# Performance work log

Measured on AMD Instinct MI355X. Metric: run time of the kernel, lower is better.

## Reference

```python
import jax, jax.numpy as jnp
import numpy as np
import math

D = 768
H = 8
DK = D // H
FF = 1024
EPS = 1e-5


def _layer_norm(x, g, b):
    m = jnp.mean(x, axis=-1, keepdims=True)
    v = jnp.mean((x - m) ** 2, axis=-1, keepdims=True)
    return (x - m) * jax.lax.rsqrt(v + EPS) * g + b


def _mha(x, attention_mask, Wq, bq, Wv, bv, g, b):
    # x: (B,S,D); attention_mask: (B,S,1) bool (True = masked/padding query row)
    B, S, _ = x.shape
    q = (x @ Wq + bq).reshape(B, S, H, DK).transpose(0, 2, 1, 3)  # (B,H,S,dk)
    # NOTE: original code uses the V projection for BOTH k and v (k = self.V(x))
    kv = (x @ Wv + bv).reshape(B, S, H, DK).transpose(0, 2, 1, 3)
    k = kv
    v = kv
    w = jnp.einsum('bhqd,bhkd->bhqk', q, k) / math.sqrt(DK)  # (B,H,S,S)
    pad = attention_mask[:, None, :, :]                      # (B,1,S,1) -> bcast (B,1,S,S)
    causal = jnp.triu(jnp.ones((S, S), dtype=bool), k=1)     # look-ahead mask
    mask = pad | causal
    w = jnp.where(mask, jnp.float32(-1e9), w)
    # NOTE: original uses nn.Softmax(dim=2) -> softmax over the QUERY axis
    score = jax.nn.softmax(w, axis=2)
    o = jnp.einsum('bhqk,bhkd->bhqd', score, v)              # (B,H,S,dk)
    o = o.transpose(0, 2, 1, 3).reshape(B, S, D)
    return _layer_norm(o + x, g, b)


def _ffn(x, W1, b1, W2, b2, g, b):
    h = jax.nn.relu(x @ W1 + b1)
    return _layer_norm(h @ W2 + b2 + x, g, b)


def setup_inputs() -> dict:
    key = jax.random.key(0)
    ks = jax.random.split(key, 16)
    B, S = 8, 1024
    sc = 0.02
    inp = {
        'x': jax.random.normal(ks[0], (B, S, D), dtype=jnp.float32),
        'attention_mask': jax.random.randint(ks[1], (B, S, 1), 0, 2).astype(bool),
    }
    for i, pre in enumerate(['a1', 'a2']):
        inp[pre + '_Wq'] = jax.random.normal(ks[2 + 4 * i], (D, D), dtype=jnp.float32) * sc
        inp[pre + '_bq'] = jnp.zeros((D,), dtype=jnp.float32)
        inp[pre + '_Wv'] = jax.random.normal(ks[3 + 4 * i], (D, D), dtype=jnp.float32) * sc
        inp[pre + '_bv'] = jnp.zeros((D,), dtype=jnp.float32)
        inp[pre + '_g'] = jnp.ones((D,), dtype=jnp.float32)
        inp[pre + '_b'] = jnp.zeros((D,), dtype=jnp.float32)
    inp['f_W1'] = jax.random.normal(ks[10], (D, FF), dtype=jnp.float32) * sc
    inp['f_b1'] = jnp.zeros((FF,), dtype=jnp.float32)
    inp['f_W2'] = jax.random.normal(ks[11], (FF, D), dtype=jnp.float32) * sc
    inp['f_b2'] = jnp.zeros((D,), dtype=jnp.float32)
    inp['f_g'] = jnp.ones((D,), dtype=jnp.float32)
    inp['f_b'] = jnp.zeros((D,), dtype=jnp.float32)
    return inp


def reference(x, attention_mask,
              a1_Wq, a1_bq, a1_Wv, a1_bv, a1_g, a1_b,
              a2_Wq, a2_bq, a2_Wv, a2_bv, a2_g, a2_b,
              f_W1, f_b1, f_W2, f_b2, f_g, f_b):
    x = _mha(x, attention_mask, a1_Wq, a1_bq, a1_Wv, a1_bv, a1_g, a1_b)
    x = _mha(x, attention_mask, a2_Wq, a2_bq, a2_Wv, a2_bv, a2_g, a2_b)
    x = _ffn(x, f_W1, f_b1, f_W2, f_b2, f_g, f_b)
    return x
```

## Files before the change

kernel.cpp:

```cpp
#include <hip/hip_runtime.h>
#include <cstddef>

#define BB 8
#define SS 1024
#define DD 768
#define HH 8
#define DKK 96
#define FFF 1024
#define MM (BB*SS)
#define QVW 1536
#define SM_SCALE 0.10206207261596577f
#define NT2 8

typedef unsigned short ushort_t;
typedef short short8 __attribute__((ext_vector_type(8)));
typedef float f32x4 __attribute__((ext_vector_type(4)));
typedef float f32x16 __attribute__((ext_vector_type(16)));
typedef ushort_t us4 __attribute__((ext_vector_type(4)));
typedef unsigned uint2v __attribute__((ext_vector_type(2)));

__device__ __forceinline__ ushort_t f2b(float f) {
    union { float f; unsigned u; } x; x.f = f;
    unsigned r = x.u + 0x7fffu + ((x.u >> 16) & 1u);
    return (ushort_t)(r >> 16);
}
__device__ __forceinline__ float b2f(ushort_t u) {
    union { unsigned u; float f; } x; x.u = ((unsigned)u) << 16;
    return x.f;
}
__device__ __forceinline__ void gload16(const ushort_t* g, void* lds_base) {
    __builtin_amdgcn_global_load_lds(
        (const __attribute__((address_space(1))) unsigned int*)g,
        (__attribute__((address_space(3))) unsigned int*)lds_base, 16, 0, 0);
}
__device__ __forceinline__ void plswap(unsigned& a, unsigned& b) {
#if __has_builtin(__builtin_amdgcn_permlane32_swap)
    uint2v r = __builtin_amdgcn_permlane32_swap(a, b, false, false);
    a = r[0]; b = r[1];
#else
    asm("v_permlane32_swap_b32 %0, %1" : "+v"(a), "+v"(b));
#endif
}

__global__ __launch_bounds__(256) void castWT(
    const float* __restrict__ W, ushort_t* __restrict__ Wt, int K, int N)
{
    __shared__ float T[32][33];
    const int tx = threadIdx.x & 31, ty = threadIdx.x >> 5;
    const int n0 = blockIdx.x * 32, k0 = blockIdx.y * 32;
    #pragma unroll
    for (int r = 0; r < 4; ++r)
        T[ty + 8*r][tx] = W[(size_t)(k0 + ty + 8*r) * N + n0 + tx];
    __syncthreads();
    #pragma unroll
    for (int r = 0; r < 4; ++r)
        Wt[(size_t)(n0 + ty + 8*r) * K + k0 + tx] = f2b(T[tx][ty + 8*r]);
}

__global__ __launch_bounds__(256) void castWT4(
    const float* __restrict__ Wa, const float* __restrict__ Wb,
    const float* __restrict__ Wc, const float* __restrict__ Wd,
    ushort_t* __restrict__ Ta, ushort_t* __restrict__ Tb,
    ushort_t* __restrict__ Tc, ushort_t* __restrict__ Td)
{
    __shared__ float T[32][33];
    const float* W; ushort_t* Wt;
    switch (blockIdx.z) {
        case 0:  W = Wa; Wt = Ta; break;
        case 1:  W = Wb; Wt = Tb; break;
        case 2:  W = Wc; Wt = Tc; break;
        default: W = Wd; Wt = Td; break;
    }
    const int tx = threadIdx.x & 31, ty = threadIdx.x >> 5;
    const int n0 = blockIdx.x * 32, k0 = blockIdx.y * 32;
    #pragma unroll
    for (int r = 0; r < 4; ++r)
        T[ty + 8*r][tx] = W[(size_t)(k0 + ty + 8*r) * DD + n0 + tx];
    __syncthreads();
    #pragma unroll
    for (int r = 0; r < 4; ++r)
        Wt[(size_t)(n0 + ty + 8*r) * DD + k0 + tx] = f2b(T[tx][ty + 8*r]);
}

__global__ __launch_bounds__(256) void cast_f2b(
    const float* __restrict__ in, ushort_t* __restrict__ out, int n4)
{
    const int i = blockIdx.x * 256 + threadIdx.x;
    if (i >= n4) return;
    const float4 v = ((const float4*)in)[i];
    us4 o; o.x = f2b(v.x); o.y = f2b(v.y); o.z = f2b(v.z); o.w = f2b(v.w);
    ((us4*)out)[i] = o;
}

template<int RELU>
__global__ __launch_bounds__(256) void gemm_bt(
    const ushort_t* __restrict__ A, const ushort_t* __restrict__ Bt,
    const float* __restrict__ bias, const float* __restrict__ bias2, int bN,
    ushort_t* __restrict__ C, int K, int N)
{
    __shared__ ushort_t S[128*136];
    ushort_t* As = S;
    ushort_t* Bs = S + 128*64;
    const int tid  = threadIdx.x;
    const int lane = tid & 63, wave = tid >> 6;
    const int wm = wave >> 1, wn = wave & 1;
    const int n = lane & 15, quad = lane >> 4;
    const int sx = n & 7;
    const int bm = blockIdx.y * 128, bn = blockIdx.x * 128;

    f32x4 acc[4][4];
    #pragma unroll
    for (int i = 0; i < 4; ++i)
        #pragma unroll
        for (int j = 0; j < 4; ++j) acc[i][j] = (f32x4){0.f, 0.f, 0.f, 0.f};

    for (int k0 = 0; k0 < K; k0 += 64) {
        #pragma unroll
        for (int it = 0; it < 4; ++it) {
            const int u   = (it*4 + wave)*64 + lane;
            const int row = u >> 3;
            const int c   = (u & 7) ^ (row & 7);
            gload16(A  + (size_t)(bm + row) * K + k0 + c*8, (char*)As + (it*4 + wave)*1024);
            gload16(Bt + (size_t)(bn + row) * K + k0 + c*8, (char*)Bs + (it*4 + wave)*1024);
        }
        __syncthreads();
        #pragma unroll
        for (int ks = 0; ks < 2; ++ks) {
            short8 af[4], bf[4];
            #pragma unroll
            for (int i = 0; i < 4; ++i)
                af[i] = *(short8*)&As[((wm*64 + i*16 + n)*8 + ((ks*4 + quad) ^ sx))*8];
            #pragma unroll
            for (int j = 0; j < 4; ++j)
                bf[j] = *(short8*)&Bs[((wn*64 + j*16 + n)*8 + ((ks*4 + quad) ^ sx))*8];
            #pragma unroll
            for (int i = 0; i < 4; ++i)
                #pragma unroll
                for (int j = 0; j < 4; ++j)
                    acc[i][j] = __builtin_amdgcn_mfma_f32_16x16x32_bf16(af[i], bf[j], acc[i][j], 0, 0, 0);
        }
        __syncthreads();
    }
    #pragma unroll
    for (int j = 0; j < 4; ++j) {
        const int col = wn*64 + j*16 + n;
        const int gcol = bn + col;
        const float bsv = (gcol < bN) ? bias[gcol] : bias2[gcol - bN];
        #pragma unroll
        for (int i = 0; i < 4; ++i) {
            const int lrow = wm*64 + i*16 + quad*4;
            #pragma unroll
            for (int r = 0; r < 4; ++r) {
                float v = acc[i][j][r] + bsv;
                if (RELU) v = fmaxf(v, 0.f);
                S[(lrow + r)*136 + col] = f2b(v);
            }
        }
    }
    __syncthreads();
    #pragma unroll
    for (int it = 0; it < 8; ++it) {
        const int u = it*256 + tid;
        const int grow = u >> 4, gc = u & 15;
        *(short8*)(C + (size_t)(bm + grow)*N + bn + gc*8) = *(short8*)&S[grow*136 + gc*8];
    }
}

__global__ __launch_bounds__(512) void attn_sums(
    const ushort_t* __restrict__ QV, const int* __restrict__ amask,
    float* __restrict__ lpart)
{
    __shared__ ushort_t Qs[128*128];
    __shared__ ushort_t Ks[2][64*128];
    __shared__ float colsum[2][8][64];
    const int tid = threadIdx.x, lane = tid & 63, wave = tid >> 6;
    const int n = lane & 15, quad = lane >> 4, sx = n & 7;
    const int hwid = blockIdx.x;
    const int v = (hwid & 7) * 32 + (hwid >> 3);
    const int px = v & 3, h = (v >> 2) & 7, b = v >> 5;
    const ushort_t* Qh = QV + (size_t)b*SS*QVW + h*DKK;
    const ushort_t* Kh = QV + (size_t)b*SS*QVW + DD + h*DKK;
    float* lpq = lpart + (size_t)(b*HH + h)*NT2*SS;

    #pragma unroll
    for (int half = 0; half < 2; ++half) {
        const int qt2 = half ? (7 - px) : px;
        const int q0 = qt2 * 128;
        const int ktmax = 2*qt2 + 1;
        #pragma unroll
        for (int it = 0; it < 4; ++it) {
            const int u = (it*8 + wave)*64 + lane;
            const int row = u >> 4, c = (u & 15) ^ (row & 7);
            if (c < 12)
                gload16(Qh + (size_t)(q0 + row)*QVW + c*8, (char*)Qs + (it*8 + wave)*1024);
        }
        const int4 mv = *(const int4*)&amask[b*SS + q0 + wave*16 + quad*4];
        const int mr[4] = {mv.x, mv.y, mv.z, mv.w};
        #pragma unroll
        for (int it = 0; it < 2; ++it) {
            const int u = (it*8 + wave)*64 + lane;
            const int row = u >> 4, c = (u & 15) ^ (row & 7);
            if (c < 12)
                gload16(Kh + (size_t)row*QVW + c*8, (char*)Ks[0] + (it*8 + wave)*1024);
        }
        __syncthreads();
        short8 aq[3];
        #pragma unroll
        for (int ks = 0; ks < 3; ++ks)
            aq[ks] = *(short8*)&Qs[((wave*16 + n)*16 + ((ks*4 + quad) ^ sx))*8];

        int cur = 0;
        for (int kt = 0; kt <= ktmax; ++kt) {
            const int k0 = kt * 64;
            if (kt < ktmax) {
                #pragma unroll
                for (int it = 0; it < 2; ++it) {
                    const int u = (it*8 + wave)*64 + lane;
                    const int row = u >> 4, c = (u & 15) ^ (row & 7);
                    if (c < 12)
                        gload16(Kh + (size_t)(k0 + 64 + row)*QVW + c*8,
                                (char*)Ks[cur^1] + (it*8 + wave)*1024);
                }
            }
            if (kt > 0 && tid < 64) {
                const float s = colsum[cur^1][0][tid] + colsum[cur^1][1][tid]
                              + colsum[cur^1][2][tid] + colsum[cur^1][3][tid]
                              + colsum[cur^1][4][tid] + colsum[cur^1][5][tid]
                              + colsum[cur^1][6][tid] + colsum[cur^1][7][tid];
                lpq[(size_t)qt2*SS + (k0 - 64) + tid] = s;
            }
            #pragma unroll
            for (int ns = 0; ns < 4; ++ns) {
                f32x4 sa = (f32x4){0.f, 0.f, 0.f, 0.f};
                #pragma unroll
                for (int ks = 0; ks < 3; ++ks) {
                    const short8 bk = *(short8*)&Ks[cur][((ns*16 + n)*16 + ((ks*4 + quad) ^ sx))*8];
                    sa = __builtin_amdgcn_mfma_f32_16x16x32_bf16(aq[ks], bk, sa, 0, 0, 0);
                }
                const int kl = ns*16 + n;
                const int keyg = k0 + kl;
                float s = 0.f;
                #pragma unroll
                for (int r = 0; r < 4; ++r) {
                    const int qg = q0 + wave*16 + quad*4 + r;
                    const bool dead = (mr[r] != 0) || (keyg > qg);
                    s += dead ? 0.f : __expf(sa[r] * SM_SCALE);
                }
                s += __shfl_xor(s, 16);
                s += __shfl_xor(s, 32);
                if (quad == 0) colsum[cur][wave][kl] = s;
            }
            __syncthreads();
            cur ^= 1;
        }
        if (tid < 64) {
            const int pb = ktmax & 1;
            const float s = colsum[pb][0][tid] + colsum[pb][1][tid]
                          + colsum[pb][2][tid] + colsum[pb][3][tid]
                          + colsum[pb][4][tid] + colsum[pb][5][tid]
                          + colsum[pb][6][tid] + colsum[pb][7][tid];
            lpq[(size_t)qt2*SS + ktmax*64 + tid] = s;
        }
    }
}

__global__ __launch_bounds__(256) void transpose_scale(
    const ushort_t* __restrict__ QV, const float* __restrict__ lpart,
    ushort_t* __restrict__ Vt)
{
    __shared__ ushort_t T[64][104];
    __shared__ float rlv[64];
    const int tid = threadIdx.x;
    const int k0 = blockIdx.x * 64, h = blockIdx.y, b = blockIdx.z;
    const ushort_t* src = QV + (size_t)b*SS*QVW + DD + h*DKK;
    for (int s = tid; s < 768; s += 256) {
        const int r = s / 12, c = s % 12;
        *(short8*)&T[r][c*8] = *(const short8*)(src + (size_t)(k0 + r)*QVW + c*8);
    }
    if (tid < 64) {
        const float* lp = lpart + (size_t)(b*HH + h)*NT2*SS;
        float l = 0.f;
        for (int qt2 = k0 >> 7; qt2 < NT2; ++qt2) l += lp[(size_t)qt2*SS + k0 + tid];
        rlv[tid] = (l > 0.f) ? (1.f / l) : 0.f;
    }
    __syncthreads();
    ushort_t* dst = Vt + ((size_t)b*HH + h)*DKK*SS;
    for (int s = tid; s < 768; s += 256) {
        const int dk = s >> 3, c = s & 7;
        short8 v;
        #pragma unroll
        for (int i = 0; i < 8; ++i)
            v[i] = (short)f2b(b2f(T[c*8 + i][dk]) * rlv[c*8 + i]);
        *(short8*)(dst + (size_t)dk*SS + k0 + c*8) = v;
    }
}

__global__ __launch_bounds__(256, 2) void attn_pv_re(
    const ushort_t* __restrict__ QV, const int* __restrict__ amask,
    const ushort_t* __restrict__ Vt, ushort_t* __restrict__ O)
{
    __shared__ ushort_t Ks[2][64*128];
    __shared__ ushort_t Vs[2][96*64];
    const int tid = threadIdx.x, lane = tid & 63, wave = tid >> 6;
    const int ln31 = lane & 31, hi = lane >> 5;
    const int hwid = blockIdx.x;
    const int v = (hwid & 7) * 32 + (hwid >> 3);
    const int px = v & 3, h = (v >> 2) & 7, b = v >> 5;
    const ushort_t* Qh = QV + (size_t)b*SS*QVW + h*DKK;
    const ushort_t* Kh = QV + (size_t)b*SS*QVW + DD + h*DKK;
    const ushort_t* Vth = Vt + ((size_t)b*HH + h)*DKK*SS;

    #pragma unroll
    for (int half = 0; half < 2; ++half) {
        const int qt2 = half ? (7 - px) : px;
        const int q0 = qt2 * 128;
        const int ktmax = 2*qt2 + 1;
        const int qrow = q0 + wave*32 + ln31;
        short8 bq[6];
        #pragma unroll
        for (int t = 0; t < 6; ++t)
            bq[t] = *(const short8*)(Qh + (size_t)qrow*QVW + t*16 + hi*8);
        const bool padq = amask[b*SS + qrow] != 0;

        #pragma unroll
        for (int it = 0; it < 4; ++it) {
            const int u = (it*4 + wave)*64 + lane;
            const int row = u >> 4, c = (u & 15) ^ (row & 7);
            if (c < 12)
                gload16(Kh + (size_t)row*QVW + c*8, (char*)Ks[0] + (it*4 + wave)*1024);
        }
        #pragma unroll
        for (int it = 0; it < 3; ++it) {
            const int u = (it*4 + wave)*64 + lane;
            const int row = u >> 3, c = (u & 7) ^ (row & 7);
            gload16(Vth + (size_t)row*SS + c*8, (char*)Vs[0] + (it*4 + wave)*1024);
        }
        __syncthreads();

        f32x16 acc[3];
        #pragma unroll
        for (int db = 0; db < 3; ++db)
            #pragma unroll
            for (int i = 0; i < 16; ++i) acc[db][i] = 0.f;

        int cur = 0;
        for (int kt = 0; kt <= ktmax; ++kt) {
            const int k0 = kt * 64;
            if (kt < ktmax) {
                #pragma unroll
                for (int it = 0; it < 4; ++it) {
                    const int u = (it*4 + wave)*64 + lane;
                    const int row = u >> 4, c = (u & 15) ^ (row & 7);
                    if (c < 12)
                        gload16(Kh + (size_t)(k0 + 64 + row)*QVW + c*8,
                                (char*)Ks[cur^1] + (it*4 + wave)*1024);
                }
                #pragma unroll
                for (int it = 0; it < 3; ++it) {
                    const int u = (it*4 + wave)*64 + lane;
                    const int row = u >> 3, c = (u & 7) ^ (row & 7);
                    gload16(Vth + (size_t)row*SS + k0 + 64 + c*8,
                            (char*)Vs[cur^1] + (it*4 + wave)*1024);
                }
            }
            #pragma unroll
            for (int kb = 0; kb < 2; ++kb) {
                f32x16 sk;
                #pragma unroll
                for (int i = 0; i < 16; ++i) sk[i] = 0.f;
                const int krow = kb*32 + ln31;
                #pragma unroll
                for (int t = 0; t < 6; ++t) {
                    const short8 ak = *(short8*)&Ks[cur][krow*128 + (((t*2 + hi) ^ (krow & 7))*8)];
                    sk = __builtin_amdgcn_mfma_f32_32x32x16_bf16(ak, bq[t], sk, 0, 0, 0);
                }
                const int kbase = k0 + kb*32 + 4*hi;
                float p[16];
                #pragma unroll
                for (int r = 0; r < 16; ++r) {
                    const int kg = kbase + (r & 3) + 8*(r >> 2);
                    const bool dead = padq || (kg > qrow);
                    p[r] = dead ? 0.f : __expf(sk[r] * SM_SCALE);
                }
                unsigned w[8];
                #pragma unroll
                for (int i = 0; i < 8; ++i)
                    asm("v_cvt_pk_bf16_f32 %0, %1, %2" : "=v"(w[i]) : "v"(p[2*i]), "v"(p[2*i+1]));
                plswap(w[0], w[2]);
                plswap(w[1], w[3]);
                plswap(w[4], w[6]);
                plswap(w[5], w[7]);
                #pragma unroll
                for (int s = 0; s < 2; ++s) {
                    short8 ae;
                    unsigned* aeu = (unsigned*)&ae;
                    aeu[0] = w[s*4 + 0]; aeu[1] = w[s*4 + 1];
                    aeu[2] = w[s*4 + 2]; aeu[3] = w[s*4 + 3];
                    #pragma unroll
                    for (int db = 0; db < 3; ++db) {
                        const int drow = db*32 + ln31;
                        const short8 bv = *(short8*)&Vs[cur][drow*64 + (((kb*4 + s*2 + hi) ^ (drow & 7))*8)];
                        acc[db] = __builtin_amdgcn_mfma_f32_32x32x16_bf16(ae, bv, acc[db], 0, 0, 0);
                    }
                }
            }
            __syncthreads();
            cur ^= 1;
        }
        #pragma unroll
        for (int db = 0; db < 3; ++db) {
            #pragma unroll
            for (int r = 0; r < 16; ++r) {
                const int q = q0 + wave*32 + (r & 3) + 8*(r >> 2) + 4*hi;
                O[((size_t)b*SS + q)*DD + h*DKK + db*32 + ln31] = f2b(acc[db][r]);
            }
        }
    }
}

__device__ __forceinline__ float block_sum256(float s, float* tmp4)
{
    #pragma unroll
    for (int off = 32; off > 0; off >>= 1) s += __shfl_down(s, off);
    __syncthreads();
    if ((threadIdx.x & 63) == 0) tmp4[threadIdx.x >> 6] = s;
    __syncthreads();
    return tmp4[0] + tmp4[1] + tmp4[2] + tmp4[3];
}

template<int XBF, int RBF, int OUTF32>
__global__ __launch_bounds__(256) void resid_ln(
    const void* __restrict__ X, const void* __restrict__ R,
    const float* __restrict__ g, const float* __restrict__ beta,
    ushort_t* __restrict__ OutB, float* __restrict__ OutF)
{
    __shared__ float tmp4[4];
    const int row = blockIdx.x;
    const int tid = threadIdx.x;
    float v[3], s = 0.f;
    #pragma unroll
    for (int i = 0; i < 3; ++i) {
        const size_t idx = (size_t)row * DD + tid + 256*i;
        const float xv = XBF ? b2f(((const ushort_t*)X)[idx]) : ((const float*)X)[idx];
        const float rv = RBF ? b2f(((const ushort_t*)R)[idx]) : ((const float*)R)[idx];
        v[i] = xv + rv;
        s += v[i];
    }
    const float mu = block_sum256(s, tmp4) * (1.f / DD);
    float qv = 0.f;
    #pragma unroll
    for (int i = 0; i < 3; ++i) { const float d = v[i] - mu; qv += d * d; }
    const float inv = rsqrtf(block_sum256(qv, tmp4) * (1.f / DD) + 1e-5f);
    #pragma unroll
    for (int i = 0; i < 3; ++i) {
        const int c = tid + 256*i;
        const float o = (v[i] - mu) * inv * g[c] + beta[c];
        if (OUTF32) OutF[(size_t)row * DD + c] = o;
        else        OutB[(size_t)row * DD + c] = f2b(o);
    }
}

extern "C" void kernel_launch(void* const* d_in, const int* in_sizes, int n_in,
                              void* d_out, int out_size, void* d_ws, size_t ws_size,
                              hipStream_t stream)
{
    (void)in_sizes; (void)n_in; (void)out_size; (void)ws_size;
    const float* x0    = (const float*)d_in[0];
    const int*   amask = (const int*)d_in[1];
    const float* a1_Wq = (const float*)d_in[2];
    const float* a1_bq = (const float*)d_in[3];
    const float* a1_Wv = (const float*)d_in[4];
    const float* a1_bv = (const float*)d_in[5];
    const float* a1_g  = (const float*)d_in[6];
    const float* a1_b  = (const float*)d_in[7];
    const float* a2_Wq = (const float*)d_in[8];
    const float* a2_bq = (const float*)d_in[9];
    const float* a2_Wv = (const float*)d_in[10];
    const float* a2_bv = (const float*)d_in[11];
    const float* a2_g  = (const float*)d_in[12];
    const float* a2_b  = (const float*)d_in[13];
    const float* f_W1  = (const float*)d_in[14];
    const float* f_b1  = (const float*)d_in[15];
    const float* f_W2  = (const float*)d_in[16];
    const float* f_b2  = (const float*)d_in[17];
    const float* f_g   = (const float*)d_in[18];
    const float* f_b   = (const float*)d_in[19];

    char* ws = (char*)d_ws;
    size_t off = 0;
    auto alloc = [&](size_t bytes) { void* p = ws + off; off += (bytes + 255) & ~(size_t)255; return p; };
    ushort_t* WqvT1 = (ushort_t*)alloc((size_t)QVW*DD*2);
    ushort_t* WqvT2 = (ushort_t*)alloc((size_t)QVW*DD*2);
    ushort_t* W1T   = (ushort_t*)alloc((size_t)DD*FFF*2);
    ushort_t* W2T   = (ushort_t*)alloc((size_t)DD*FFF*2);
    ushort_t* xb0   = (ushort_t*)alloc((size_t)MM*DD*2);
    ushort_t* xb1   = (ushort_t*)alloc((size_t)MM*DD*2);
    ushort_t* xb2   = (ushort_t*)alloc((size_t)MM*DD*2);
    ushort_t* Ob    = (ushort_t*)alloc((size_t)MM*DD*2);
    ushort_t* QVb   = (ushort_t*)alloc((size_t)MM*QVW*2);
    ushort_t* hb    = QVb;
    ushort_t* Vtb   = (ushort_t*)alloc((size_t)MM*DD*2);
    float* lpart = (float*)alloc((size_t)BB*HH*NT2*SS*4);
    float* out = (float*)d_out;

    const dim3 blk(256);
    const dim3 blk512(512);
    const dim3 gat(256);
    const dim3 gtr(SS/64, HH, BB);
    const dim3 gqv(QVW/128, MM/128);
    const dim3 gf1(FFF/128, MM/128);
    const dim3 gf2(DD/128, MM/128);

    castWT4<<<dim3(DD/32, DD/32, 4), blk, 0, stream>>>(
        a1_Wq, a1_Wv, a2_Wq, a2_Wv,
        WqvT1, WqvT1 + (size_t)DD*DD, WqvT2, WqvT2 + (size_t)DD*DD);
    castWT<<<dim3(FFF/32, DD/32), blk, 0, stream>>>(f_W1, W1T, DD, FFF);
    castWT<<<dim3(DD/32, FFF/32), blk, 0, stream>>>(f_W2, W2T, FFF, DD);
    cast_f2b<<<(MM*DD/4 + 255)/256, blk, 0, stream>>>(x0, xb0, MM*DD/4);

    gemm_bt<0><<<gqv, blk, 0, stream>>>(xb0, WqvT1, a1_bq, a1_bv, DD, QVb, DD, QVW);
    attn_sums<<<gat, blk512, 0, stream>>>(QVb, amask, lpart);
    transpose_scale<<<gtr, blk, 0, stream>>>(QVb, lpart, Vtb);
    attn_pv_re<<<gat, blk, 0, stream>>>(QVb, amask, Vtb, Ob);
    resid_ln<1,0,0><<<dim3(MM), blk, 0, stream>>>(Ob, x0, a1_g, a1_b, xb1, nullptr);

    gemm_bt<0><<<gqv, blk, 0, stream>>>(xb1, WqvT2, a2_bq, a2_bv, DD, QVb, DD, QVW);
    attn_sums<<<gat, blk512, 0, stream>>>(QVb, amask, lpart);
    transpose_scale<<<gtr, blk, 0, stream>>>(QVb, lpart, Vtb);
    attn_pv_re<<<gat, blk, 0, stream>>>(QVb, amask, Vtb, Ob);
    resid_ln<1,1,0><<<dim3(MM), blk, 0, stream>>>(Ob, xb1, a2_g, a2_b, xb2, nullptr);

    gemm_bt<1><<<gf1, blk, 0, stream>>>(xb2, W1T, f_b1, f_b1, FFF, hb, DD, FFF);
    gemm_bt<0><<<gf2, blk, 0, stream>>>(hb, W2T, f_b2, f_b2, DD, Ob, FFF, DD);
    resid_ln<1,1,1><<<dim3(MM), blk, 0, stream>>>(Ob, xb2, f_g, f_b, nullptr, out);
}
```

Measured before the change: 409.0 us.

## Merge prep kernels, swizzle GEMM block order across XCDs, raise MFMA priority

Folds the four weight/input cast kernels into one launch, saving launch gaps. GEMMs switch to a 1D grid remapped so consecutive tiles land on the same XCD, aiming at better L2 reuse of A/B panels. MFMA sections in the GEMM and both attention kernels are wrapped in s_setprio to favour matrix issue over other waves. Together these are independent tweaks whose benefits are modest and depend on scheduling behaviour.

Measured after the change: 382.7 us. 6.4% less time.

```diff
diff --git a/kernel.cpp b/kernel.cpp
--- a/kernel.cpp
+++ b/kernel.cpp
@@ -42,12 +42,13 @@
 #endif
 }
 
-__global__ __launch_bounds__(256) void castWT(
-    const float* __restrict__ W, ushort_t* __restrict__ Wt, int K, int N)
+__device__ __forceinline__ void castWT_body(
+    const float* __restrict__ W, ushort_t* __restrict__ Wt,
+    int K, int N, int bx, int by)
 {
     __shared__ float T[32][33];
     const int tx = threadIdx.x & 31, ty = threadIdx.x >> 5;
-    const int n0 = blockIdx.x * 32, k0 = blockIdx.y * 32;
+    const int n0 = bx * 32, k0 = by * 32;
     #pragma unroll
     for (int r = 0; r < 4; ++r)
         T[ty + 8*r][tx] = W[(size_t)(k0 + ty + 8*r) * N + n0 + tx];
@@ -57,39 +58,33 @@
         Wt[(size_t)(n0 + ty + 8*r) * K + k0 + tx] = f2b(T[tx][ty + 8*r]);
 }
 
-__global__ __launch_bounds__(256) void castWT4(
-    const float* __restrict__ Wa, const float* __restrict__ Wb,
-    const float* __restrict__ Wc, const float* __restrict__ Wd,
-    ushort_t* __restrict__ Ta, ushort_t* __restrict__ Tb,
-    ushort_t* __restrict__ Tc, ushort_t* __restrict__ Td)
-{
-    __shared__ float T[32][33];
-    const float* W; ushort_t* Wt;
-    switch (blockIdx.z) {
-        case 0:  W = Wa; Wt = Ta; break;
-        case 1:  W = Wb; Wt = Tb; break;
-        case 2:  W = Wc; Wt = Tc; break;
-        default: W = Wd; Wt = Td; break;
-    }
-    const int tx = threadIdx.x & 31, ty = threadIdx.x >> 5;
-    const int n0 = blockIdx.x * 32, k0 = blockIdx.y * 32;
-    #pragma unroll
-    for (int r = 0; r < 4; ++r)
-        T[ty + 8*r][tx] = W[(size_t)(k0 + ty + 8*r) * DD + n0 + tx];
-    __syncthreads();
-    #pragma unroll
-    for (int r = 0; r < 4; ++r)
-        Wt[(size_t)(n0 + ty + 8*r) * DD + k0 + tx] = f2b(T[tx][ty + 8*r]);
-}
-
-__global__ __launch_bounds__(256) void cast_f2b(
-    const float* __restrict__ in, ushort_t* __restrict__ out, int n4)
-{
-    const int i = blockIdx.x * 256 + threadIdx.x;
-    if (i >= n4) return;
-    const float4 v = ((const float4*)in)[i];
-    us4 o; o.x = f2b(v.x); o.y = f2b(v.y); o.z = f2b(v.z); o.w = f2b(v.w);
-    ((us4*)out)[i] = o;
+__global__ __launch_bounds__(256) void prep_all(
+    const float* __restrict__ Wqa, const float* __restrict__ Wva,
+    const float* __restrict__ Wqb, const float* __restrict__ Wvb,
+    ushort_t* __restrict__ Tqa, ushort_t* __restrict__ Tva,
+    ushort_t* __restrict__ Tqb, ushort_t* __restrict__ Tvb,
+    const float* __restrict__ W1, ushort_t* __restrict__ T1,
+    const float* __restrict__ W2, ushort_t* __restrict__ T2,
+    const float* __restrict__ x, ushort_t* __restrict__ xb)
+{
+    const int id = blockIdx.x;
+    if (id < 2304) {
+        const int z = id / 576, r = id % 576;
+        const float* W = (z == 0) ? Wqa : (z == 1) ? Wva : (z == 2) ? Wqb : Wvb;
+        ushort_t* Wt   = (z == 0) ? Tqa : (z == 1) ? Tva : (z == 2) ? Tqb : Tvb;
+        castWT_body(W, Wt, DD, DD, r % 24, r / 24);
+    } else if (id < 3072) {
+        const int r = id - 2304;
+        castWT_body(W1, T1, DD, FFF, r % 32, r / 32);
+    } else if (id < 3840) {
+        const int r = id - 3072;
+        castWT_body(W2, T2, FFF, DD, r % 24, r / 24);
+    } else {
+        const int i = (id - 3840) * 256 + threadIdx.x;
+        const float4 v = ((const float4*)x)[i];
+        us4 o; o.x = f2b(v.x); o.y = f2b(v.y); o.z = f2b(v.z); o.w = f2b(v.w);
+        ((us4*)xb)[i] = o;
+    }
 }
 
 template<int RELU>
@@ -106,7 +101,10 @@
     const int wm = wave >> 1, wn = wave & 1;
     const int n = lane & 15, quad = lane >> 4;
     const int sx = n & 7;
-    const int bm = blockIdx.y * 128, bn = blockIdx.x * 128;
+    const int nbx = N >> 7;
+    const int cpx = gridDim.x >> 3;
+    const int sw  = (blockIdx.x & 7) * cpx + (blockIdx.x >> 3);
+    const int bm = (sw / nbx) * 128, bn = (sw % nbx) * 128;
 
     f32x4 acc[4][4];
     #pragma unroll
@@ -133,11 +131,13 @@
             #pragma unroll
             for (int j = 0; j < 4; ++j)
                 bf[j] = *(short8*)&Bs[((wn*64 + j*16 + n)*8 + ((ks*4 + quad) ^ sx))*8];
+            __builtin_amdgcn_s_setprio(1);
             #pragma unroll
             for (int i = 0; i < 4; ++i)
                 #pragma unroll
                 for (int j = 0; j < 4; ++j)
                     acc[i][j] = __builtin_amdgcn_mfma_f32_16x16x32_bf16(af[i], bf[j], acc[i][j], 0, 0, 0);
+            __builtin_amdgcn_s_setprio(0);
         }
         __syncthreads();
     }
@@ -232,11 +232,13 @@
             #pragma unroll
             for (int ns = 0; ns < 4; ++ns) {
                 f32x4 sa = (f32x4){0.f, 0.f, 0.f, 0.f};
+                __builtin_amdgcn_s_setprio(1);
                 #pragma unroll
                 for (int ks = 0; ks < 3; ++ks) {
                     const short8 bk = *(short8*)&Ks[cur][((ns*16 + n)*16 + ((ks*4 + quad) ^ sx))*8];
                     sa = __builtin_amdgcn_mfma_f32_16x16x32_bf16(aq[ks], bk, sa, 0, 0, 0);
                 }
+                __builtin_amdgcn_s_setprio(0);
                 const int kl = ns*16 + n;
                 const int keyg = k0 + kl;
                 float s = 0.f;
@@ -369,11 +371,13 @@
                 #pragma unroll
                 for (int i = 0; i < 16; ++i) sk[i] = 0.f;
                 const int krow = kb*32 + ln31;
+                __builtin_amdgcn_s_setprio(1);
                 #pragma unroll
                 for (int t = 0; t < 6; ++t) {
                     const short8 ak = *(short8*)&Ks[cur][krow*128 + (((t*2 + hi) ^ (krow & 7))*8)];
                     sk = __builtin_amdgcn_mfma_f32_32x32x16_bf16(ak, bq[t], sk, 0, 0, 0);
                 }
+                __builtin_amdgcn_s_setprio(0);
                 const int kbase = k0 + kb*32 + 4*hi;
                 float p[16];
                 #pragma unroll
@@ -390,6 +394,7 @@
                 plswap(w[1], w[3]);
                 plswap(w[4], w[6]);
                 plswap(w[5], w[7]);
+                __builtin_amdgcn_s_setprio(1);
                 #pragma unroll
                 for (int s = 0; s < 2; ++s) {
                     short8 ae;
@@ -403,6 +408,7 @@
                         acc[db] = __builtin_amdgcn_mfma_f32_32x32x16_bf16(ae, bv, acc[db], 0, 0, 0);
                     }
                 }
+                __builtin_amdgcn_s_setprio(0);
             }
             __syncthreads();
             cur ^= 1;
@@ -507,30 +513,25 @@
     const dim3 blk512(512);
     const dim3 gat(256);
     const dim3 gtr(SS/64, HH, BB);
-    const dim3 gqv(QVW/128, MM/128);
-    const dim3 gf1(FFF/128, MM/128);
-    const dim3 gf2(DD/128, MM/128);
-
-    castWT4<<<dim3(DD/32, DD/32, 4), blk, 0, stream>>>(
+
+    prep_all<<<dim3(9984), blk, 0, stream>>>(
         a1_Wq, a1_Wv, a2_Wq, a2_Wv,
-        WqvT1, WqvT1 + (size_t)DD*DD, WqvT2, WqvT2 + (size_t)DD*DD);
-    castWT<<<dim3(FFF/32, DD/32), blk, 0, stream>>>(f_W1, W1T, DD, FFF);
-    castWT<<<dim3(DD/32, FFF/32), blk, 0, stream>>>(f_W2, W2T, FFF, DD);
-    cast_f2b<<<(MM*DD/4 + 255)/256, blk, 0, stream>>>(x0, xb0, MM*DD/4);
-
-    gemm_bt<0><<<gqv, blk, 0, stream>>>(xb0, WqvT1, a1_bq, a1_bv, DD, QVb, DD, QVW);
+        WqvT1, WqvT1 + (size_t)DD*DD, WqvT2, WqvT2 + (size_t)DD*DD,
+        f_W1, W1T, f_W2, W2T, x0, xb0);
+
+    gemm_bt<0><<<dim3((QVW/128)*(MM/128)), blk, 0, stream>>>(xb0, WqvT1, a1_bq, a1_bv, DD, QVb, DD, QVW);
     attn_sums<<<gat, blk512, 0, stream>>>(QVb, amask, lpart);
     transpose_scale<<<gtr, blk, 0, stream>>>(QVb, lpart, Vtb);
     attn_pv_re<<<gat, blk, 0, stream>>>(QVb, amask, Vtb, Ob);
     resid_ln<1,0,0><<<dim3(MM), blk, 0, stream>>>(Ob, x0, a1_g, a1_b, xb1, nullptr);
 
-    gemm_bt<0><<<gqv, blk, 0, stream>>>(xb1, WqvT2, a2_bq, a2_bv, DD, QVb, DD, QVW);
+    gemm_bt<0><<<dim3((QVW/128)*(MM/128)), blk, 0, stream>>>(xb1, WqvT2, a2_bq, a2_bv, DD, QVb, DD, QVW);
     attn_sums<<<gat, blk512, 0, stream>>>(QVb, amask, lpart);
     transpose_scale<<<gtr, blk, 0, stream>>>(QVb, lpart, Vtb);
     attn_pv_re<<<gat, blk, 0, stream>>>(QVb, amask, Vtb, Ob);
     resid_ln<1,1,0><<<dim3(MM), blk, 0, stream>>>(Ob, xb1, a2_g, a2_b, xb2, nullptr);
 
-    gemm_bt<1><<<gf1, blk, 0, stream>>>(xb2, W1T, f_b1, f_b1, FFF, hb, DD, FFF);
-    gemm_bt<0><<<gf2, blk, 0, stream>>>(hb, W2T, f_b2, f_b2, DD, Ob, FFF, DD);
+    gemm_bt<1><<<dim3((FFF/128)*(MM/128)), blk, 0, stream>>>(xb2, W1T, f_b1, f_b1, FFF, hb, DD, FFF);
+    gemm_bt<0><<<dim3((DD/128)*(MM/128)), blk, 0, stream>>>(hb, W2T, f_b2, f_b2, DD, Ob, FFF, DD);
     resid_ln<1,1,1><<<dim3(MM), blk, 0, stream>>>(Ob, xb2, f_g, f_b, nullptr, out);
 }
```
